# Performance work log

Hardware: AMD Instinct MI355X
Metric: run time of the kernel (lower is better)

The kernel has to match this reference:

```python
import jax, jax.numpy as jnp
import numpy as np

N_HEAD = 16

def setup_inputs() -> dict:
    key = jax.random.key(0)
    k1, k2, k3 = jax.random.split(key, 3)
    B, K, C = 2, 2048, 1024
    x = jax.random.normal(k1, (B, K, C), dtype=jnp.float32)
    W_qkv = jax.random.normal(k2, (C, 3 * C), dtype=jnp.float32) * (1.0 / np.sqrt(C))
    b_qkv = jnp.zeros((3 * C,), dtype=jnp.float32)
    W_proj = jax.random.normal(k3, (C, C), dtype=jnp.float32) * (1.0 / np.sqrt(C))
    b_proj = jnp.zeros((C,), dtype=jnp.float32)
    return {"x": x, "W_qkv": W_qkv, "b_qkv": b_qkv, "W_proj": W_proj, "b_proj": b_proj, "K": K}

def reference(x, W_qkv, b_qkv, W_proj, b_proj, K):
    B, _, C = x.shape
    H = N_HEAD
    Dh = C // H
    qkv = x @ W_qkv + b_qkv                      # [B, K, 3C]
    q, k, v = jnp.split(qkv, 3, axis=-1)
    # [B, H, K, Dh]
    q = q.reshape(B, K, H, Dh).transpose(0, 2, 1, 3)
    k = k.reshape(B, K, H, Dh).transpose(0, 2, 1, 3)
    v = v.reshape(B, K, H, Dh).transpose(0, 2, 1, 3)
    att = jnp.einsum('bhqd,bhkd->bhqk', q, k) / jnp.sqrt(jnp.asarray(Dh, dtype=x.dtype))
    causal = jnp.tril(jnp.ones((K, K), dtype=bool))
    att = jnp.where(causal[None, None], att, jnp.asarray(-jnp.inf, dtype=x.dtype))
    att = jax.nn.softmax(att, axis=-1)
    y = jnp.einsum('bhqk,bhkd->bhqd', att, v)    # [B, H, K, Dh]
    y = y.transpose(0, 2, 1, 3).reshape(B, K, C)
    return y @ W_proj + b_proj
```

## Files before the change

kernel.cpp:

```cpp
#include <hip/hip_runtime.h>
#include <hip/hip_bf16.h>
#include <math.h>

typedef __attribute__((ext_vector_type(8))) short short8;
typedef __attribute__((ext_vector_type(4))) float f32x4;
typedef __attribute__((ext_vector_type(4))) short short4v;
typedef __attribute__((ext_vector_type(2))) int int2v;

static __device__ __forceinline__ short f2bf(float f) {
    __hip_bfloat16 h = __float2bfloat16(f);
    return *reinterpret_cast<short*>(&h);
}
static __device__ __forceinline__ void store_out(float* p, float v) { *p = v; }
static __device__ __forceinline__ void store_out(short* p, float v) { *p = f2bf(v); }

#define GLL16(g, l) __builtin_amdgcn_global_load_lds( \
    (const __attribute__((address_space(1))) void*)(g), \
    (__attribute__((address_space(3))) void*)(l), 16, 0, 0)

#if __has_builtin(__builtin_amdgcn_exp2f)
#define EXP2(x) __builtin_amdgcn_exp2f(x)
#else
#define EXP2(x) exp2f(x)
#endif

#if __has_builtin(__builtin_amdgcn_cvt_pk_bf16_f32)
typedef __attribute__((ext_vector_type(2))) __bf16 bf16x2;
static __device__ __forceinline__ int pack2bf(float a, float b) {
    bf16x2 r = __builtin_amdgcn_cvt_pk_bf16_f32(a, b);
    return __builtin_bit_cast(int, r);
}
#else
static __device__ __forceinline__ int pack2bf(float a, float b) {
    unsigned ua = __builtin_bit_cast(unsigned, a) + 0x8000u;
    unsigned ub = __builtin_bit_cast(unsigned, b) + 0x8000u;
    return (int)((ua >> 16) | (ub & 0xFFFF0000u));
}
#endif

static __device__ __forceinline__ void transpose_cast_tile(
    const float* __restrict__ W, short* __restrict__ Wt, int Kd, int N,
    int bx, int by)
{
    __shared__ float ts[32][33];
    const int c0 = bx * 32, r0 = by * 32;
    const int tx = threadIdx.x & 31, ty = threadIdx.x >> 5;
    #pragma unroll
    for (int e = 0; e < 4; ++e)
        ts[ty + e * 8][tx] = W[(size_t)(r0 + ty + e * 8) * N + c0 + tx];
    __syncthreads();
    #pragma unroll
    for (int e = 0; e < 4; ++e)
        Wt[(size_t)(c0 + ty + e * 8) * Kd + r0 + tx] = f2bf(ts[tx][ty + e * 8]);
}

__global__ __launch_bounds__(256) void prep_kernel(
    const float* __restrict__ x,      short* __restrict__ xb,    int nx,
    const float* __restrict__ W_qkv,  short* __restrict__ Wt1,
    const float* __restrict__ W_proj, short* __restrict__ Wt2,
    int C)
{
    const int nbx = nx / 1024;
    const int nb1 = (3 * C / 32) * (C / 32);
    int bid = blockIdx.x;
    if (bid < nbx) {
        int i = (bid * 256 + threadIdx.x) * 4;
        float4 v = *(const float4*)(x + i);
        short4v o = { f2bf(v.x), f2bf(v.y), f2bf(v.z), f2bf(v.w) };
        *(short4v*)(xb + i) = o;
        return;
    }
    bid -= nbx;
    if (bid < nb1) {
        const int nc = 3 * C / 32;
        transpose_cast_tile(W_qkv, Wt1, C, 3 * C, bid % nc, bid / nc);
        return;
    }
    bid -= nb1;
    {
        const int nc = C / 32;
        transpose_cast_tile(W_proj, Wt2, C, C, bid % nc, bid / nc);
    }
}

__global__ __launch_bounds__(256) void kvpack_kernel(
    const short* __restrict__ qkvb, short* __restrict__ kvp, int K, int C)
{
    __shared__ __attribute__((aligned(16))) short Ks[64][80];
    __shared__ __attribute__((aligned(16))) short Vs[64][76];
    const int k0 = blockIdx.x * 64, h = blockIdx.y, b = blockIdx.z;
    const size_t rs = (size_t)3 * C;
    const short* kb = qkvb + (size_t)b * K * rs + C + h * 64;
    const short* vb = qkvb + (size_t)b * K * rs + 2 * C + h * 64;
    const int key = threadIdx.x >> 3, d0 = (threadIdx.x & 7) * 8;

    *(short8*)&Ks[key][d0]      = *(const short8*)(kb + (size_t)(k0 + key) * rs + d0);
    *(short8*)&Ks[key + 32][d0] = *(const short8*)(kb + (size_t)(k0 + key + 32) * rs + d0);
    short8 v0 = *(const short8*)(vb + (size_t)(k0 + key) * rs + d0);
    short8 v1 = *(const short8*)(vb + (size_t)(k0 + key + 32) * rs + d0);
    *(short4v*)&Vs[key][d0]          = __builtin_shufflevector(v0, v0, 0, 1, 2, 3);
    *(short4v*)&Vs[key][d0 + 4]      = __builtin_shufflevector(v0, v0, 4, 5, 6, 7);
    *(short4v*)&Vs[key + 32][d0]     = __builtin_shufflevector(v1, v1, 0, 1, 2, 3);
    *(short4v*)&Vs[key + 32][d0 + 4] = __builtin_shufflevector(v1, v1, 4, 5, 6, 7);
    __syncthreads();

    const int bh = b * 16 + h;
    #pragma unroll
    for (int ss = 0; ss < 2; ++ss) {
        const int s    = threadIdx.x + ss * 256;
        const int ci_l = s >> 8, f = (s >> 6) & 3, lane = s & 63;
        const int col  = lane & 15, quad = lane >> 4;
        const int ci   = (k0 >> 5) + ci_l;
        const size_t cb = ((size_t)bh * 64 + ci) * 4096;
        {
            const int nb = f >> 1, half = f & 1;
            short8 d = *(const short8*)&Ks[ci_l * 32 + 2 * col + nb][quad * 8 + half * 32];
            *(short8*)(kvp + cb + (size_t)f * 512 + lane * 8) = d;
        }
        {
            const int db = f;
            short8 d;
            #pragma unroll
            for (int j = 0; j < 8; ++j)
                d[j] = Vs[ci_l * 32 + quad * 8 + j][db * 16 + col];
            *(short8*)(kvp + cb + (size_t)(4 + db) * 512 + lane * 8) = d;
        }
    }
}

#define GK 32

template <typename OutT, int GM, int GN>
__global__ __launch_bounds__(256) void gemm_mfma_kernel(
    const short* __restrict__ A, const short* __restrict__ Bt,
    const float* __restrict__ bias, OutT* __restrict__ C,
    int M, int N, int Kd, int qcols, float qscale)
{
    constexpr int WM = GM / 2, WN = GN / 2;
    __shared__ __attribute__((aligned(16))) short As[GM * GK];
    __shared__ __attribute__((aligned(16))) short Bs[GN * GK];
    const int tid  = threadIdx.x;
    const int lane = tid & 63, w = tid >> 6;
    const int col  = lane & 15, quad = lane >> 4;
    const int wm = (w & 1) * WM, wn = (w >> 1) * WN;
    const int row0 = blockIdx.y * GM, col0 = blockIdx.x * GN;
    const float sc = (col0 < qcols) ? qscale : 1.f;

    const int sr = tid >> 2, scg = (tid & 3) * 8;
    const short* gA = A  + (size_t)(row0 + sr) * Kd + scg;
    const short* gB = Bt + (size_t)(col0 + sr) * Kd + scg;
    short* lA = As + sr * GK + scg;
    short* lB = Bs + sr * GK + scg;
    const size_t skip = (size_t)64 * Kd;

    f32x4 acc[WM / 16][WN / 16] = {};
    for (int k0 = 0; k0 < Kd; k0 += GK) {
        __syncthreads();
        #pragma unroll
        for (int t = 0; t < GM / 64; ++t) GLL16(gA + t * skip, lA + t * 64 * GK);
        #pragma unroll
        for (int t = 0; t < GN / 64; ++t) GLL16(gB + t * skip, lB + t * 64 * GK);
        gA += GK; gB += GK;
        __syncthreads();

        short8 aF[WM / 16], bF[WN / 16];
        #pragma unroll
        for (int mt = 0; mt < WM / 16; ++mt)
            aF[mt] = *(const short8*)&As[(wm + mt * 16 + col) * GK + quad * 8];
        #pragma unroll
        for (int nt = 0; nt < WN / 16; ++nt)
            bF[nt] = *(const short8*)&Bs[(wn + nt * 16 + col) * GK + quad * 8];
        #pragma unroll
        for (int mt = 0; mt < WM / 16; ++mt)
            #pragma unroll
            for (int nt = 0; nt < WN / 16; ++nt)
                acc[mt][nt] = __builtin_amdgcn_mfma_f32_16x16x32_bf16(aF[mt], bF[nt], acc[mt][nt], 0, 0, 0);
    }

    #pragma unroll
    for (int mt = 0; mt < WM / 16; ++mt)
        #pragma unroll
        for (int i = 0; i < 4; ++i) {
            const size_t r = row0 + wm + mt * 16 + quad * 4 + i;
            #pragma unroll
            for (int nt = 0; nt < WN / 16; ++nt) {
                const int c = col0 + wn + nt * 16 + col;
                store_out(&C[r * N + c], (acc[mt][nt][i] + bias[c]) * sc);
            }
        }
}

#define DH 64

__global__ __launch_bounds__(256, 4) void flash_mfma_kernel(
    const short* __restrict__ qkvb,
    const short* __restrict__ kvp,
    short* __restrict__ y,
    int K, int C)
{
    __shared__ __attribute__((aligned(16))) short smem[8704];

    const int tid  = threadIdx.x;
    const int lane = tid & 63, w = tid >> 6;
    const int col  = lane & 15, quad = lane >> 4;

    short* Pw = smem + w * 1280;

    const int cmb = blockIdx.x & 31;
    const int g   = blockIdx.x >> 5;
    const int b   = cmb >> 4, h = cmb & 15;

    short8 bOnes;
    #pragma unroll
    for (int j = 0; j < 8; ++j) bOnes[j] = (col == 0) ? (short)0x3F80 : (short)0;

    const size_t rs = (size_t)3 * C;
    const short* qbase  = qkvb + (size_t)b * K * rs + h * DH;
    const short* kvbase = kvp + (size_t)cmb * 64 * 4096 + lane * 8;

    struct Frag { short8 k[2][2]; short8 v[4]; };
    auto loadF = [&](Frag& f, int ci) {
        const short* p = kvbase + (size_t)ci * 4096;
        f.k[0][0] = *(const short8*)(p);
        f.k[0][1] = *(const short8*)(p + 512);
        f.k[1][0] = *(const short8*)(p + 1024);
        f.k[1][1] = *(const short8*)(p + 1536);
        f.v[0]    = *(const short8*)(p + 2048);
        f.v[1]    = *(const short8*)(p + 2560);
        f.v[2]    = *(const short8*)(p + 3072);
        f.v[3]    = *(const short8*)(p + 3584);
    };

    auto run = [&](int T) {
        const int t0 = T * 32;
        const int NC = T + 1;

        short8 aQ[2][2];
        #pragma unroll
        for (int qg = 0; qg < 2; ++qg) {
            const short* qp = qbase + (size_t)(t0 + qg * 16 + col) * rs;
            aQ[qg][0] = *(const short8*)(qp + quad * 8);
            aQ[qg][1] = *(const short8*)(qp + 32 + quad * 8);
        }
        f32x4 O[2][4] = {};
        f32x4 L4[2] = {};

        for (int ci = w; ci < NC; ci += 4) {
            Frag f;
            loadF(f, ci);
            const int kc = ci * 32;
            __builtin_amdgcn_s_setprio(1);
            #pragma unroll
            for (int qg = 0; qg < 2; ++qg) {
                const int qb = t0 + qg * 16;
                short* Ptq = Pw + qg * 640;
                f32x4 S[2] = {};
                #pragma unroll
                for (int nb = 0; nb < 2; ++nb) {
                    S[nb] = __builtin_amdgcn_mfma_f32_16x16x32_bf16(aQ[qg][0], f.k[nb][0], S[nb], 0, 0, 0);
                    S[nb] = __builtin_amdgcn_mfma_f32_16x16x32_bf16(aQ[qg][1], f.k[nb][1], S[nb], 0, 0, 0);
                }
                if (kc + 31 <= qb) {
                    #pragma unroll
                    for (int i = 0; i < 4; ++i)
                        *(int*)&Ptq[(quad * 4 + i) * 40 + col * 2] =
                            pack2bf(EXP2(S[0][i]), EXP2(S[1][i]));
                } else {
                    const int kg = kc + col * 2;
                    #pragma unroll
                    for (int i = 0; i < 4; ++i) {
                        const int q = qb + quad * 4 + i;
                        float s0 = (kg + 0 <= q) ? S[0][i] : -INFINITY;
                        float s1 = (kg + 1 <= q) ? S[1][i] : -INFINITY;
                        *(int*)&Ptq[(quad * 4 + i) * 40 + col * 2] =
                            pack2bf(EXP2(s0), EXP2(s1));
                    }
                }
                short8 aP = *(const short8*)&Ptq[col * 40 + quad * 8];
                #pragma unroll
                for (int db = 0; db < 4; ++db)
                    O[qg][db] = __builtin_amdgcn_mfma_f32_16x16x32_bf16(aP, f.v[db], O[qg][db], 0, 0, 0);
                L4[qg] = __builtin_amdgcn_mfma_f32_16x16x32_bf16(aP, bOnes, L4[qg], 0, 0, 0);
            }
            __builtin_amdgcn_s_setprio(0);
        }

        float* OrA = (float*)smem;
        float* OrB = OrA + 32 * 68;
        __syncthreads();
        if (w < 2) {
            float* R = (w == 0) ? OrA : OrB;
            #pragma unroll
            for (int qg = 0; qg < 2; ++qg)
                #pragma unroll
                for (int i = 0; i < 4; ++i) {
                    const int row = qg * 16 + quad * 4 + i;
                    #pragma unroll
                    for (int db = 0; db < 4; ++db)
                        R[row * 68 + db * 16 + col] = O[qg][db][i];
                    if (col == 0) R[row * 68 + 64] = L4[qg][i];
                }
        }
        __syncthreads();
        if (w >= 2) {
            float* R = (w == 2) ? OrA : OrB;
            #pragma unroll
            for (int qg = 0; qg < 2; ++qg)
                #pragma unroll
                for (int i = 0; i < 4; ++i) {
                    const int row = qg * 16 + quad * 4 + i;
                    #pragma unroll
                    for (int db = 0; db < 4; ++db)
                        R[row * 68 + db * 16 + col] += O[qg][db][i];
                    if (col == 0) R[row * 68 + 64] += L4[qg][i];
                }
        }
        __syncthreads();

        #pragma unroll
        for (int rstep = 0; rstep < 2; ++rstep) {
            const int row = w * 8 + rstep * 4 + quad;
            f32x4 oa = *(const f32x4*)&OrA[row * 68 + col * 4];
            f32x4 ob = *(const f32x4*)&OrB[row * 68 + col * 4];
            const float inv = 1.f / (OrA[row * 68 + 64] + OrB[row * 68 + 64]);
            int2v o2 = { pack2bf((oa[0] + ob[0]) * inv, (oa[1] + ob[1]) * inv),
                         pack2bf((oa[2] + ob[2]) * inv, (oa[3] + ob[3]) * inv) };
            *(int2v*)(y + ((size_t)b * K + t0 + row) * C + h * DH + col * 4) = o2;
        }
        __syncthreads();
    };

    run(g);
    run(63 - g);
}

extern "C" void kernel_launch(void* const* d_in, const int* in_sizes, int n_in,
                              void* d_out, int out_size, void* d_ws, size_t ws_size,
                              hipStream_t stream)
{
    const float* x      = (const float*)d_in[0];
    const float* W_qkv  = (const float*)d_in[1];
    const float* b_qkv  = (const float*)d_in[2];
    const float* W_proj = (const float*)d_in[3];
    const float* b_proj = (const float*)d_in[4];

    const int B = 2, K = 2048, C = 1024, H = 16;
    const int M = B * K;
    const float C2 = 0.18033688f;

    char* ws = (char*)d_ws;
    short* xb    = (short*)ws;  ws += (size_t)M * C * 2;
    short* Wt1   = (short*)ws;  ws += (size_t)3 * C * C * 2;
    short* Wt2   = (short*)ws;  ws += (size_t)C * C * 2;
    short* qkvb  = (short*)ws;  ws += (size_t)M * 3 * C * 2;
    short* yb    = (short*)ws;  ws += (size_t)M * C * 2;
    short* kvp   = (short*)ws;

    const int nbx = (M * C) / 1024;
    const int nb1 = (3 * C / 32) * (C / 32);
    const int nb2 = (C / 32) * (C / 32);
    prep_kernel<<<nbx + nb1 + nb2, 256, 0, stream>>>(x, xb, M * C, W_qkv, Wt1, W_proj, Wt2, C);

    dim3 g1((3 * C) / 128, M / 128);
    gemm_mfma_kernel<short, 128, 128><<<g1, 256, 0, stream>>>(xb, Wt1, b_qkv, qkvb, M, 3 * C, C, C, C2);

    dim3 gv(K / 64, H, B);
    kvpack_kernel<<<gv, 256, 0, stream>>>(qkvb, kvp, K, C);

    flash_mfma_kernel<<<dim3(32 * 32), 256, 0, stream>>>(qkvb, kvp, yb, K, C);

    dim3 g3(C / 64, M / 128);
    gemm_mfma_kernel<float, 128, 64><<<g3, 256, 0, stream>>>(yb, Wt2, b_proj, (float*)d_out, M, C, C, 0, 1.f);
}
```

Measured before the change: 180.2 us.

## Software-pipeline attention loop: overlap next chunk's QK/exp with current PV

Splits each key/value chunk's fragment load into separate K and V loads. The loop is restructured so the QK^T score and exp for chunk n+1 are issued before the PV MFMAs of chunk n, with P fragments ping-ponged between two register sets. The goal is to hide global load latency and exp/LDS work behind MFMA execution. It also drops the s_setprio hints and raises register pressure, which may reduce occupancy.

Measured after the change: 326.8 us. +81.3%, slower.

```diff
diff --git a/kernel.cpp b/kernel.cpp
--- a/kernel.cpp
+++ b/kernel.cpp
@@ -218,17 +218,21 @@
     const short* qbase  = qkvb + (size_t)b * K * rs + h * DH;
     const short* kvbase = kvp + (size_t)cmb * 64 * 4096 + lane * 8;
 
-    struct Frag { short8 k[2][2]; short8 v[4]; };
-    auto loadF = [&](Frag& f, int ci) {
+    struct KF { short8 k[2][2]; };
+    struct VF { short8 v[4]; };
+    auto loadK = [&](KF& f, int ci) {
         const short* p = kvbase + (size_t)ci * 4096;
         f.k[0][0] = *(const short8*)(p);
         f.k[0][1] = *(const short8*)(p + 512);
         f.k[1][0] = *(const short8*)(p + 1024);
         f.k[1][1] = *(const short8*)(p + 1536);
-        f.v[0]    = *(const short8*)(p + 2048);
-        f.v[1]    = *(const short8*)(p + 2560);
-        f.v[2]    = *(const short8*)(p + 3072);
-        f.v[3]    = *(const short8*)(p + 3584);
+    };
+    auto loadV = [&](VF& f, int ci) {
+        const short* p = kvbase + (size_t)ci * 4096 + 2048;
+        f.v[0] = *(const short8*)(p);
+        f.v[1] = *(const short8*)(p + 512);
+        f.v[2] = *(const short8*)(p + 1024);
+        f.v[3] = *(const short8*)(p + 1536);
     };
 
     auto run = [&](int T) {
@@ -245,11 +249,8 @@
         f32x4 O[2][4] = {};
         f32x4 L4[2] = {};
 
-        for (int ci = w; ci < NC; ci += 4) {
-            Frag f;
-            loadF(f, ci);
+        auto sexp = [&](const KF& f, int ci, short8 (&aP)[2]) {
             const int kc = ci * 32;
-            __builtin_amdgcn_s_setprio(1);
             #pragma unroll
             for (int qg = 0; qg < 2; ++qg) {
                 const int qb = t0 + qg * 16;
@@ -276,13 +277,38 @@
                             pack2bf(EXP2(s0), EXP2(s1));
                     }
                 }
-                short8 aP = *(const short8*)&Ptq[col * 40 + quad * 8];
+                aP[qg] = *(const short8*)&Ptq[col * 40 + quad * 8];
+            }
+        };
+        auto pv = [&](const short8 (&aP)[2], const VF& f) {
+            #pragma unroll
+            for (int qg = 0; qg < 2; ++qg) {
                 #pragma unroll
                 for (int db = 0; db < 4; ++db)
-                    O[qg][db] = __builtin_amdgcn_mfma_f32_16x16x32_bf16(aP, f.v[db], O[qg][db], 0, 0, 0);
-                L4[qg] = __builtin_amdgcn_mfma_f32_16x16x32_bf16(aP, bOnes, L4[qg], 0, 0, 0);
+                    O[qg][db] = __builtin_amdgcn_mfma_f32_16x16x32_bf16(aP[qg], f.v[db], O[qg][db], 0, 0, 0);
+                L4[qg] = __builtin_amdgcn_mfma_f32_16x16x32_bf16(aP[qg], bOnes, L4[qg], 0, 0, 0);
             }
-            __builtin_amdgcn_s_setprio(0);
+        };
+
+        int ci = w;
+        if (ci < NC) {
+            KF kf; VF vf;
+            short8 aPA[2], aPB[2];
+            loadK(kf, ci);
+            sexp(kf, ci, aPA);
+            for (;;) {
+                int cn = ci + 4;
+                if (cn >= NC) { loadV(vf, ci); pv(aPA, vf); break; }
+                loadV(vf, ci); loadK(kf, cn);
+                sexp(kf, cn, aPB);
+                pv(aPA, vf);
+                ci = cn; cn += 4;
+                if (cn >= NC) { loadV(vf, ci); pv(aPB, vf); break; }
+                loadV(vf, ci); loadK(kf, cn);
+                sexp(kf, cn, aPA);
+                pv(aPB, vf);
+                ci = cn;
+            }
         }
 
         float* OrA = (float*)smem;
```

## Fuse K/V fragment packing into QKV GEMM epilogue, drop kvpack kernel

Applied to the files above, without the earlier changes.

The QKV projection GEMM now writes Q straight to a compact Q buffer and, for K and V column tiles, stages the tile in LDS (V transposed) and writes it directly into the MFMA-fragment packed layout the flash kernel reads. This removes the separate kvpack launch and the round trip through the full qkv buffer in global memory. In exchange the GEMM epilogue gains extra LDS traffic and another barrier, plus more shared memory per block.

Measured after the change: 177.0 us. No clear change (-1.8%).

```diff
diff --git a/kernel.cpp b/kernel.cpp
--- a/kernel.cpp
+++ b/kernel.cpp
@@ -83,58 +83,116 @@
     }
 }
 
-__global__ __launch_bounds__(256) void kvpack_kernel(
-    const short* __restrict__ qkvb, short* __restrict__ kvp, int K, int C)
-{
-    __shared__ __attribute__((aligned(16))) short Ks[64][80];
-    __shared__ __attribute__((aligned(16))) short Vs[64][76];
-    const int k0 = blockIdx.x * 64, h = blockIdx.y, b = blockIdx.z;
-    const size_t rs = (size_t)3 * C;
-    const short* kb = qkvb + (size_t)b * K * rs + C + h * 64;
-    const short* vb = qkvb + (size_t)b * K * rs + 2 * C + h * 64;
-    const int key = threadIdx.x >> 3, d0 = (threadIdx.x & 7) * 8;
-
-    *(short8*)&Ks[key][d0]      = *(const short8*)(kb + (size_t)(k0 + key) * rs + d0);
-    *(short8*)&Ks[key + 32][d0] = *(const short8*)(kb + (size_t)(k0 + key + 32) * rs + d0);
-    short8 v0 = *(const short8*)(vb + (size_t)(k0 + key) * rs + d0);
-    short8 v1 = *(const short8*)(vb + (size_t)(k0 + key + 32) * rs + d0);
-    *(short4v*)&Vs[key][d0]          = __builtin_shufflevector(v0, v0, 0, 1, 2, 3);
-    *(short4v*)&Vs[key][d0 + 4]      = __builtin_shufflevector(v0, v0, 4, 5, 6, 7);
-    *(short4v*)&Vs[key + 32][d0]     = __builtin_shufflevector(v1, v1, 0, 1, 2, 3);
-    *(short4v*)&Vs[key + 32][d0 + 4] = __builtin_shufflevector(v1, v1, 4, 5, 6, 7);
+#define GK 32
+
+__global__ __launch_bounds__(256) void gemm_qkv_kernel(
+    const short* __restrict__ A, const short* __restrict__ Bt,
+    const float* __restrict__ bias,
+    short* __restrict__ qb, short* __restrict__ kvp,
+    int M, int N, int Kd, int C, int Ktok, float qscale)
+{
+    __shared__ __attribute__((aligned(16))) short smem[17408];
+    short* As = smem;
+    short* Bs = smem + 4096;
+    short* T  = smem;
+
+    const int tid  = threadIdx.x;
+    const int lane = tid & 63, w = tid >> 6;
+    const int col  = lane & 15, quad = lane >> 4;
+    const int wm = (w & 1) * 64, wn = (w >> 1) * 64;
+    const int row0 = blockIdx.y * 128, col0 = blockIdx.x * 128;
+
+    const int sr = tid >> 2, scg = (tid & 3) * 8;
+    const short* gA = A  + (size_t)(row0 + sr) * Kd + scg;
+    const short* gB = Bt + (size_t)(col0 + sr) * Kd + scg;
+    short* lA = As + sr * GK + scg;
+    short* lB = Bs + sr * GK + scg;
+    const size_t skip = (size_t)64 * Kd;
+
+    f32x4 acc[4][4] = {};
+    for (int k0 = 0; k0 < Kd; k0 += GK) {
+        __syncthreads();
+        GLL16(gA,        lA);
+        GLL16(gA + skip, lA + 64 * GK);
+        GLL16(gB,        lB);
+        GLL16(gB + skip, lB + 64 * GK);
+        gA += GK; gB += GK;
+        __syncthreads();
+
+        short8 aF[4], bF[4];
+        #pragma unroll
+        for (int mt = 0; mt < 4; ++mt)
+            aF[mt] = *(const short8*)&As[(wm + mt * 16 + col) * GK + quad * 8];
+        #pragma unroll
+        for (int nt = 0; nt < 4; ++nt)
+            bF[nt] = *(const short8*)&Bs[(wn + nt * 16 + col) * GK + quad * 8];
+        #pragma unroll
+        for (int mt = 0; mt < 4; ++mt)
+            #pragma unroll
+            for (int nt = 0; nt < 4; ++nt)
+                acc[mt][nt] = __builtin_amdgcn_mfma_f32_16x16x32_bf16(aF[mt], bF[nt], acc[mt][nt], 0, 0, 0);
+    }
+
+    if (col0 < C) {
+        #pragma unroll
+        for (int mt = 0; mt < 4; ++mt)
+            #pragma unroll
+            for (int i = 0; i < 4; ++i) {
+                const size_t r = row0 + wm + mt * 16 + quad * 4 + i;
+                #pragma unroll
+                for (int nt = 0; nt < 4; ++nt) {
+                    const int c = col0 + wn + nt * 16 + col;
+                    qb[r * C + c] = f2bf((acc[mt][nt][i] + bias[c]) * qscale);
+                }
+            }
+        return;
+    }
+
+    const bool isK = col0 < 2 * C;
     __syncthreads();
-
-    const int bh = b * 16 + h;
-    #pragma unroll
-    for (int ss = 0; ss < 2; ++ss) {
-        const int s    = threadIdx.x + ss * 256;
-        const int ci_l = s >> 8, f = (s >> 6) & 3, lane = s & 63;
-        const int col  = lane & 15, quad = lane >> 4;
-        const int ci   = (k0 >> 5) + ci_l;
-        const size_t cb = ((size_t)bh * 64 + ci) * 4096;
-        {
+    #pragma unroll
+    for (int mt = 0; mt < 4; ++mt)
+        #pragma unroll
+        for (int i = 0; i < 4; ++i) {
+            const int rr = wm + mt * 16 + quad * 4 + i;
+            #pragma unroll
+            for (int nt = 0; nt < 4; ++nt) {
+                const int cr = wn + nt * 16 + col;
+                const short v = f2bf(acc[mt][nt][i] + bias[col0 + cr]);
+                if (isK) T[rr * 136 + cr] = v;
+                else     T[cr * 136 + rr] = v;
+            }
+        }
+    __syncthreads();
+
+    const int bb  = row0 / Ktok, k0t = row0 % Ktok;
+    const int h0  = (col0 - (isK ? C : 2 * C)) >> 6;
+    #pragma unroll
+    for (int j = 0; j < 8; ++j) {
+        const int s     = tid + j * 256;
+        const int lane2 = s & 63, f = (s >> 6) & 3, cil = (s >> 8) & 3, hl = s >> 10;
+        const int col2  = lane2 & 15, quad2 = lane2 >> 4;
+        short8 d;
+        if (isK) {
             const int nb = f >> 1, half = f & 1;
-            short8 d = *(const short8*)&Ks[ci_l * 32 + 2 * col + nb][quad * 8 + half * 32];
-            *(short8*)(kvp + cb + (size_t)f * 512 + lane * 8) = d;
-        }
-        {
-            const int db = f;
-            short8 d;
-            #pragma unroll
-            for (int j = 0; j < 8; ++j)
-                d[j] = Vs[ci_l * 32 + quad * 8 + j][db * 16 + col];
-            *(short8*)(kvp + cb + (size_t)(4 + db) * 512 + lane * 8) = d;
-        }
-    }
-}
-
-#define GK 32
+            d = *(const short8*)&T[(cil * 32 + 2 * col2 + nb) * 136
+                                   + hl * 64 + half * 32 + quad2 * 8];
+        } else {
+            d = *(const short8*)&T[(hl * 64 + f * 16 + col2) * 136
+                                   + cil * 32 + quad2 * 8];
+        }
+        const int bh = bb * 16 + h0 + hl;
+        const int ci = (k0t >> 5) + cil;
+        const int fr = isK ? f : 4 + f;
+        *(short8*)(kvp + (((size_t)bh * 64 + ci) * 8 + fr) * 512 + lane2 * 8) = d;
+    }
+}
 
 template <typename OutT, int GM, int GN>
 __global__ __launch_bounds__(256) void gemm_mfma_kernel(
     const short* __restrict__ A, const short* __restrict__ Bt,
     const float* __restrict__ bias, OutT* __restrict__ C,
-    int M, int N, int Kd, int qcols, float qscale)
+    int M, int N, int Kd)
 {
     constexpr int WM = GM / 2, WN = GN / 2;
     __shared__ __attribute__((aligned(16))) short As[GM * GK];
@@ -144,7 +202,6 @@
     const int col  = lane & 15, quad = lane >> 4;
     const int wm = (w & 1) * WM, wn = (w >> 1) * WN;
     const int row0 = blockIdx.y * GM, col0 = blockIdx.x * GN;
-    const float sc = (col0 < qcols) ? qscale : 1.f;
 
     const int sr = tid >> 2, scg = (tid & 3) * 8;
     const short* gA = A  + (size_t)(row0 + sr) * Kd + scg;
@@ -185,7 +242,7 @@
             #pragma unroll
             for (int nt = 0; nt < WN / 16; ++nt) {
                 const int c = col0 + wn + nt * 16 + col;
-                store_out(&C[r * N + c], (acc[mt][nt][i] + bias[c]) * sc);
+                store_out(&C[r * N + c], acc[mt][nt][i] + bias[c]);
             }
         }
 }
@@ -193,7 +250,7 @@
 #define DH 64
 
 __global__ __launch_bounds__(256, 4) void flash_mfma_kernel(
-    const short* __restrict__ qkvb,
+    const short* __restrict__ qb,
     const short* __restrict__ kvp,
     short* __restrict__ y,
     int K, int C)
@@ -214,8 +271,7 @@
     #pragma unroll
     for (int j = 0; j < 8; ++j) bOnes[j] = (col == 0) ? (short)0x3F80 : (short)0;
 
-    const size_t rs = (size_t)3 * C;
-    const short* qbase  = qkvb + (size_t)b * K * rs + h * DH;
+    const short* qbase  = qb + (size_t)b * K * C + h * DH;
     const short* kvbase = kvp + (size_t)cmb * 64 * 4096 + lane * 8;
 
     struct Frag { short8 k[2][2]; short8 v[4]; };
@@ -238,7 +294,7 @@
         short8 aQ[2][2];
         #pragma unroll
         for (int qg = 0; qg < 2; ++qg) {
-            const short* qp = qbase + (size_t)(t0 + qg * 16 + col) * rs;
+            const short* qp = qbase + (size_t)(t0 + qg * 16 + col) * C;
             aQ[qg][0] = *(const short8*)(qp + quad * 8);
             aQ[qg][1] = *(const short8*)(qp + 32 + quad * 8);
         }
@@ -252,7 +308,7 @@
             __builtin_amdgcn_s_setprio(1);
             #pragma unroll
             for (int qg = 0; qg < 2; ++qg) {
-                const int qb = t0 + qg * 16;
+                const int qb2 = t0 + qg * 16;
                 short* Ptq = Pw + qg * 640;
                 f32x4 S[2] = {};
                 #pragma unroll
@@ -260,7 +316,7 @@
                     S[nb] = __builtin_amdgcn_mfma_f32_16x16x32_bf16(aQ[qg][0], f.k[nb][0], S[nb], 0, 0, 0);
                     S[nb] = __builtin_amdgcn_mfma_f32_16x16x32_bf16(aQ[qg][1], f.k[nb][1], S[nb], 0, 0, 0);
                 }
-                if (kc + 31 <= qb) {
+                if (kc + 31 <= qb2) {
                     #pragma unroll
                     for (int i = 0; i < 4; ++i)
                         *(int*)&Ptq[(quad * 4 + i) * 40 + col * 2] =
@@ -269,7 +325,7 @@
                     const int kg = kc + col * 2;
                     #pragma unroll
                     for (int i = 0; i < 4; ++i) {
-                        const int q = qb + quad * 4 + i;
+                        const int q = qb2 + quad * 4 + i;
                         float s0 = (kg + 0 <= q) ? S[0][i] : -INFINITY;
                         float s1 = (kg + 1 <= q) ? S[1][i] : -INFINITY;
                         *(int*)&Ptq[(quad * 4 + i) * 40 + col * 2] =
@@ -352,7 +408,7 @@
     short* xb    = (short*)ws;  ws += (size_t)M * C * 2;
     short* Wt1   = (short*)ws;  ws += (size_t)3 * C * C * 2;
     short* Wt2   = (short*)ws;  ws += (size_t)C * C * 2;
-    short* qkvb  = (short*)ws;  ws += (size_t)M * 3 * C * 2;
+    short* qb    = (short*)ws;  ws += (size_t)M * C * 2;
     short* yb    = (short*)ws;  ws += (size_t)M * C * 2;
     short* kvp   = (short*)ws;
 
@@ -362,13 +418,10 @@
     prep_kernel<<<nbx + nb1 + nb2, 256, 0, stream>>>(x, xb, M * C, W_qkv, Wt1, W_proj, Wt2, C);
 
     dim3 g1((3 * C) / 128, M / 128);
-    gemm_mfma_kernel<short, 128, 128><<<g1, 256, 0, stream>>>(xb, Wt1, b_qkv, qkvb, M, 3 * C, C, C, C2);
-
-    dim3 gv(K / 64, H, B);
-    kvpack_kernel<<<gv, 256, 0, stream>>>(qkvb, kvp, K, C);
-
-    flash_mfma_kernel<<<dim3(32 * 32), 256, 0, stream>>>(qkvb, kvp, yb, K, C);
+    gemm_qkv_kernel<<<g1, 256, 0, stream>>>(xb, Wt1, b_qkv, qb, kvp, M, 3 * C, C, C, K, C2);
+
+    flash_mfma_kernel<<<dim3(32 * 32), 256, 0, stream>>>(qb, kvp, yb, K, C);
 
     dim3 g3(C / 64, M / 128);
-    gemm_mfma_kernel<float, 128, 64><<<g3, 256, 0, stream>>>(yb, Wt2, b_proj, (float*)d_out, M, C, C, 0, 1.f);
-}
+    gemm_mfma_kernel<float, 128, 64><<<g3, 256, 0, stream>>>(yb, Wt2, b_proj, (float*)d_out, M, C, C);
+}
```
